# Performance work log

Hardware: AMD Instinct MI355X
Metric: run time of the kernel (lower is better)

## Reference

```python
import jax, jax.numpy as jnp
import numpy as np

NEG_INF_DIAG = 1000000.0

def setup_inputs() -> dict:
    key = jax.random.key(0)
    k1, k2, k3 = jax.random.split(key, 3)
    B, N, S, D = 64, 32, 256, 128
    return {
        "query_embeddings": jax.random.normal(k1, (B, N, D), dtype=jnp.float32),
        "doc_embeddings": jax.random.normal(k2, (B, S, D), dtype=jnp.float32),
        "neg_doc_embeddings": jax.random.normal(k3, (B, S, D), dtype=jnp.float32),
    }

def _maxsim(q, d):
    # q: (b, n, dim), d: (b, s, dim) -> (b,) sum over n of max over s of q.d
    return jnp.einsum('bnd,bsd->bns', q, d).max(axis=2).sum(axis=1)

def reference(query_embeddings, doc_embeddings, neg_doc_embeddings):
    pos_scores = _maxsim(query_embeddings, doc_embeddings)
    neg_scores = _maxsim(query_embeddings, neg_doc_embeddings)
    loss = jax.nn.softplus(neg_scores - pos_scores).mean()

    # in-batch term: scores[b, c] = MaxSim(query b, doc c)
    scores = jnp.einsum('bnd,csd->bcns', query_embeddings, doc_embeddings).max(axis=3).sum(axis=2)  # (B, B)
    pos = jnp.diagonal(scores)
    B = scores.shape[0]
    neg = (scores - jnp.eye(B, dtype=scores.dtype) * NEG_INF_DIAG).max(axis=1)
    loss = loss + jax.nn.softplus(neg - pos).mean()
    return loss / 2
```

## Files before the change

### kernel.cpp

```cpp
#include <hip/hip_runtime.h>
#include <hip/hip_bf16.h>

#define B_SZ 64
#define N_Q 32

typedef __attribute__((ext_vector_type(8))) short bf16x8;
typedef __attribute__((ext_vector_type(4))) float f32x4;

static __device__ __forceinline__ unsigned short f2bf(float f) {
    __hip_bfloat16 h = __float2bfloat16(f);
    return *reinterpret_cast<unsigned short*>(&h);
}

static __device__ __forceinline__ bf16x8 cvt_frag(const float* __restrict__ src) {
    float4 a = reinterpret_cast<const float4*>(src)[0];
    float4 b = reinterpret_cast<const float4*>(src)[1];
    union { bf16x8 v; unsigned short u[8]; } t;
    t.u[0] = f2bf(a.x); t.u[1] = f2bf(a.y); t.u[2] = f2bf(a.z); t.u[3] = f2bf(a.w);
    t.u[4] = f2bf(b.x); t.u[5] = f2bf(b.y); t.u[6] = f2bf(b.z); t.u[7] = f2bf(b.w);
    return t.v;
}

#define MFMA(A, Bv, C) __builtin_amdgcn_mfma_f32_16x16x32_bf16(A, Bv, C, 0, 0, 0)

__global__ __launch_bounds__(256) void cvt_permute(const float* __restrict__ q,
                                                   const float* __restrict__ dd,
                                                   const float* __restrict__ nd,
                                                   unsigned short* __restrict__ DP,
                                                   unsigned short* __restrict__ QP) {
    const int blk = blockIdx.x, tid = threadIdx.x;
    if (blk < 2048) {
        const int o = blk * 256 + tid;
        const int doc = o >> 12;
        const int u = o & 4095;
        const int ln = u & 63, nt = (u >> 6) & 3, kk = (u >> 8) & 3, ch = u >> 10;
        const int s  = ch * 64 + nt * 16 + (ln & 15);
        const int k0 = kk * 32 + (ln >> 4) * 8;
        const float* src = ((doc < 64) ? (dd + (size_t)doc * 32768)
                                       : (nd + (size_t)(doc - 64) * 32768)) + s * 128 + k0;
        reinterpret_cast<bf16x8*>(DP)[o] = cvt_frag(src);
    } else {
        const int g = (blk - 2048) * 256 + tid;
        const int b = g >> 9, u = g & 511;
        const int ln = u & 63, mt = (u >> 6) & 1, kk = u >> 7;
        const int n  = mt * 16 + (ln & 15);
        const int k0 = kk * 32 + (ln >> 4) * 8;
        reinterpret_cast<bf16x8*>(QP)[g] = cvt_frag(q + (size_t)b * 4096 + n * 128 + k0);
    }
}

__global__ __launch_bounds__(256, 2) void maxsim_kernel(const unsigned short* __restrict__ QP,
                                                        const unsigned short* __restrict__ DP,
                                                        float* __restrict__ scores) {
    const int wg  = blockIdx.x;
    const int tid = threadIdx.x;
    const int wave = tid >> 6, lane = tid & 63;
    const int l15 = lane & 15;

    __shared__ bf16x8 docB[4096];
    __shared__ float wredN[4][4][8];

    const bf16x8* DP8 = reinterpret_cast<const bf16x8*>(DP);
    const bf16x8* QP8 = reinterpret_cast<const bf16x8*>(QP);

    int c, b;
    bool isNeg;
    if (wg < 1024) { c = wg >> 4; b = (wg & 15) * 4 + wave; isNeg = false; }
    else           { b = wg - 1024; c = b; isNeg = true; }
    const int dcc = isNeg ? (64 + b) : c;

    bf16x8 Af[4][2];
    const bf16x8* qsrc = QP8 + (size_t)b * 512 + lane;
    #pragma unroll
    for (int kk = 0; kk < 4; ++kk) {
        Af[kk][0] = qsrc[kk * 128];
        Af[kk][1] = qsrc[kk * 128 + 64];
    }

    const bf16x8* dsrc = DP8 + (size_t)dcc * 4096 + wave * 1024 + lane;
    #pragma unroll
    for (int f = 0; f < 16; ++f)
        docB[wave * 1024 + f * 64 + lane] = dsrc[f * 64];
    __syncthreads();

    float rmax[2][4];
    #pragma unroll
    for (int mt = 0; mt < 2; ++mt)
        #pragma unroll
        for (int r = 0; r < 4; ++r) rmax[mt][r] = -3.0e38f;

    const int nch = isNeg ? 1 : 4;
    for (int i = 0; i < nch; ++i) {
        const int ch = isNeg ? wave : ((wave + i) & 3);
        f32x4 acc[2][4] = {};
        #pragma unroll
        for (int kk = 0; kk < 4; ++kk) {
            #pragma unroll
            for (int nt = 0; nt < 4; ++nt) {
                bf16x8 Bv = docB[ch * 1024 + kk * 256 + nt * 64 + lane];
                acc[0][nt] = MFMA(Af[kk][0], Bv, acc[0][nt]);
                acc[1][nt] = MFMA(Af[kk][1], Bv, acc[1][nt]);
            }
        }
        #pragma unroll
        for (int mt = 0; mt < 2; ++mt)
            #pragma unroll
            for (int r = 0; r < 4; ++r)
                rmax[mt][r] = fmaxf(rmax[mt][r],
                    fmaxf(fmaxf(acc[mt][0][r], acc[mt][1][r]),
                          fmaxf(acc[mt][2][r], acc[mt][3][r])));
    }

    float part = 0.0f;
    #pragma unroll
    for (int mt = 0; mt < 2; ++mt)
        #pragma unroll
        for (int r = 0; r < 4; ++r) {
            float m = rmax[mt][r];
            m = fmaxf(m, __shfl_xor(m, 1, 64));
            m = fmaxf(m, __shfl_xor(m, 2, 64));
            m = fmaxf(m, __shfl_xor(m, 4, 64));
            m = fmaxf(m, __shfl_xor(m, 8, 64));
            if (isNeg) {
                if (l15 == 0) wredN[wave][lane >> 4][mt * 4 + r] = m;
            } else {
                part += m;
            }
        }
    if (!isNeg) {
        part += __shfl_xor(part, 16, 64);
        part += __shfl_xor(part, 32, 64);
        if (lane == 0) scores[(size_t)b * 65 + c] = part;
    } else {
        __syncthreads();
        if (tid < 32) {
            const int l4v = tid >> 3, slot = tid & 7;
            float m = fmaxf(fmaxf(wredN[0][l4v][slot], wredN[1][l4v][slot]),
                            fmaxf(wredN[2][l4v][slot], wredN[3][l4v][slot]));
            m += __shfl_xor(m, 1, 64);
            m += __shfl_xor(m, 2, 64);
            m += __shfl_xor(m, 4, 64);
            m += __shfl_xor(m, 8, 64);
            m += __shfl_xor(m, 16, 64);
            if (tid == 0) scores[(size_t)b * 65 + 64] = m;
        }
    }
}

static __device__ __forceinline__ float softplusf(float x) {
    return fmaxf(x, 0.0f) + log1pf(expf(-fabsf(x)));
}

__global__ __launch_bounds__(64) void loss_kernel(const float* __restrict__ scores,
                                                  float* __restrict__ out) {
    const int b = threadIdx.x;
    const float* row = scores + b * 65;
    const float pos  = row[b];
    const float negq = row[64];
    float nib = -1e30f;
    #pragma unroll
    for (int c = 0; c < B_SZ; ++c) {
        float v = row[c] - ((c == b) ? 1000000.0f : 0.0f);
        nib = fmaxf(nib, v);
    }
    float t = softplusf(negq - pos) + softplusf(nib - pos);
    t += __shfl_xor(t, 1, 64);
    t += __shfl_xor(t, 2, 64);
    t += __shfl_xor(t, 4, 64);
    t += __shfl_xor(t, 8, 64);
    t += __shfl_xor(t, 16, 64);
    t += __shfl_xor(t, 32, 64);
    if (b == 0) out[0] = t * (0.5f / 64.0f);
}

extern "C" void kernel_launch(void* const* d_in, const int* in_sizes, int n_in,
                              void* d_out, int out_size, void* d_ws, size_t ws_size,
                              hipStream_t stream) {
    const float* q  = (const float*)d_in[0];
    const float* dd = (const float*)d_in[1];
    const float* nd = (const float*)d_in[2];
    float* out = (float*)d_out;

    unsigned short* DP = (unsigned short*)d_ws;
    unsigned short* QP = DP + (size_t)128 * 32768;
    float* scores = (float*)(QP + (size_t)64 * 4096);

    cvt_permute<<<2176, 256, 0, stream>>>(q, dd, nd, DP, QP);

    maxsim_kernel<<<1024 + B_SZ, 256, 0, stream>>>(QP, DP, scores);

    loss_kernel<<<1, 64, 0, stream>>>(scores, out);
}
```

Before: 88.18 us.

## Fuse fp32-to-bf16 conversion into maxsim kernel with two queries per wave

Drops the separate cvt_permute pass. The maxsim kernel now reads fp32 queries and documents directly, converts them to bf16 in registers and writes documents into a swizzled LDS layout. Each wave handles two queries, so the grid halves and every LDS doc fragment feeds twice as many MFMAs. The negative-doc blocks now run all four chunks redundantly per wave and keep only one result. Risks are uncoalesced strided fp32 loads, redundant conversion of the same document across 8 blocks, and higher register pressure.

```diff
diff --git a/kernel.cpp b/kernel.cpp
--- a/kernel.cpp
+++ b/kernel.cpp
@@ -2,7 +2,6 @@
 #include <hip/hip_bf16.h>
 
 #define B_SZ 64
-#define N_Q 32
 
 typedef __attribute__((ext_vector_type(8))) short bf16x8;
 typedef __attribute__((ext_vector_type(4))) float f32x4;
@@ -23,127 +22,105 @@
 
 #define MFMA(A, Bv, C) __builtin_amdgcn_mfma_f32_16x16x32_bf16(A, Bv, C, 0, 0, 0)
 
-__global__ __launch_bounds__(256) void cvt_permute(const float* __restrict__ q,
-                                                   const float* __restrict__ dd,
-                                                   const float* __restrict__ nd,
-                                                   unsigned short* __restrict__ DP,
-                                                   unsigned short* __restrict__ QP) {
-    const int blk = blockIdx.x, tid = threadIdx.x;
-    if (blk < 2048) {
-        const int o = blk * 256 + tid;
-        const int doc = o >> 12;
-        const int u = o & 4095;
-        const int ln = u & 63, nt = (u >> 6) & 3, kk = (u >> 8) & 3, ch = u >> 10;
-        const int s  = ch * 64 + nt * 16 + (ln & 15);
-        const int k0 = kk * 32 + (ln >> 4) * 8;
-        const float* src = ((doc < 64) ? (dd + (size_t)doc * 32768)
-                                       : (nd + (size_t)(doc - 64) * 32768)) + s * 128 + k0;
-        reinterpret_cast<bf16x8*>(DP)[o] = cvt_frag(src);
-    } else {
-        const int g = (blk - 2048) * 256 + tid;
-        const int b = g >> 9, u = g & 511;
-        const int ln = u & 63, mt = (u >> 6) & 1, kk = u >> 7;
-        const int n  = mt * 16 + (ln & 15);
-        const int k0 = kk * 32 + (ln >> 4) * 8;
-        reinterpret_cast<bf16x8*>(QP)[g] = cvt_frag(q + (size_t)b * 4096 + n * 128 + k0);
-    }
-}
-
-__global__ __launch_bounds__(256, 2) void maxsim_kernel(const unsigned short* __restrict__ QP,
-                                                        const unsigned short* __restrict__ DP,
+__global__ __launch_bounds__(256, 2) void maxsim_kernel(const float* __restrict__ q,
+                                                        const float* __restrict__ dd,
+                                                        const float* __restrict__ nd,
                                                         float* __restrict__ scores) {
-    const int wg  = blockIdx.x;
-    const int tid = threadIdx.x;
+    const int idx = blockIdx.x, tid = threadIdx.x;
     const int wave = tid >> 6, lane = tid & 63;
-    const int l15 = lane & 15;
+    const int l15 = lane & 15, l4 = lane >> 4;
 
     __shared__ bf16x8 docB[4096];
-    __shared__ float wredN[4][4][8];
 
-    const bf16x8* DP8 = reinterpret_cast<const bf16x8*>(DP);
-    const bf16x8* QP8 = reinterpret_cast<const bf16x8*>(QP);
-
-    int c, b;
-    bool isNeg;
-    if (wg < 1024) { c = wg >> 4; b = (wg & 15) * 4 + wave; isNeg = false; }
-    else           { b = wg - 1024; c = b; isNeg = true; }
-    const int dcc = isNeg ? (64 + b) : c;
-
-    bf16x8 Af[4][2];
-    const bf16x8* qsrc = QP8 + (size_t)b * 512 + lane;
-    #pragma unroll
-    for (int kk = 0; kk < 4; ++kk) {
-        Af[kk][0] = qsrc[kk * 128];
-        Af[kk][1] = qsrc[kk * 128 + 64];
+    int b0, b1, ccol;
+    const float* docf;
+    if (idx < 512) {
+        const int c = idx >> 3, g = idx & 7;
+        b0 = g * 8 + wave * 2; b1 = b0 + 1; ccol = c;
+        docf = dd + (size_t)c * 32768;
+    } else {
+        b0 = b1 = idx - 512; ccol = B_SZ;
+        docf = nd + (size_t)b0 * 32768;
     }
 
-    const bf16x8* dsrc = DP8 + (size_t)dcc * 4096 + wave * 1024 + lane;
+    bf16x8 Af[2][4][2];
     #pragma unroll
-    for (int f = 0; f < 16; ++f)
-        docB[wave * 1024 + f * 64 + lane] = dsrc[f * 64];
+    for (int kk = 0; kk < 4; ++kk)
+        #pragma unroll
+        for (int mt = 0; mt < 2; ++mt) {
+            const int off = (mt * 16 + l15) * 128 + kk * 32 + l4 * 8;
+            Af[0][kk][mt] = cvt_frag(q + (size_t)b0 * 4096 + off);
+            Af[1][kk][mt] = cvt_frag(q + (size_t)b1 * 4096 + off);
+        }
+
+    {
+        const float* dsrc = docf + wave * 8192;
+        #pragma unroll
+        for (int f = 0; f < 16; ++f) {
+            const int s_local = f * 4 + l4;
+            const int kc = l15;
+            bf16x8 v = cvt_frag(dsrc + s_local * 128 + kc * 8);
+            const int logical = wave * 1024 + (kc >> 2) * 256 + (s_local >> 4) * 64
+                                + (kc & 3) * 16 + (s_local & 15);
+            docB[logical ^ ((kc >> 2) << 1)] = v;
+        }
+    }
     __syncthreads();
 
-    float rmax[2][4];
+    float rmax[2][2][4];
     #pragma unroll
-    for (int mt = 0; mt < 2; ++mt)
+    for (int qi = 0; qi < 2; ++qi)
         #pragma unroll
-        for (int r = 0; r < 4; ++r) rmax[mt][r] = -3.0e38f;
+        for (int mt = 0; mt < 2; ++mt)
+            #pragma unroll
+            for (int r = 0; r < 4; ++r) rmax[qi][mt][r] = -3.0e38f;
 
-    const int nch = isNeg ? 1 : 4;
-    for (int i = 0; i < nch; ++i) {
-        const int ch = isNeg ? wave : ((wave + i) & 3);
-        f32x4 acc[2][4] = {};
+    #pragma unroll
+    for (int i = 0; i < 4; ++i) {
+        const int ch = (wave + i) & 3;
+        f32x4 acc[2][2][4] = {};
         #pragma unroll
         for (int kk = 0; kk < 4; ++kk) {
+            const int rbase = ch * 1024 + kk * 256 + (lane ^ (kk << 1));
             #pragma unroll
             for (int nt = 0; nt < 4; ++nt) {
-                bf16x8 Bv = docB[ch * 1024 + kk * 256 + nt * 64 + lane];
-                acc[0][nt] = MFMA(Af[kk][0], Bv, acc[0][nt]);
-                acc[1][nt] = MFMA(Af[kk][1], Bv, acc[1][nt]);
+                bf16x8 Bv = docB[rbase + nt * 64];
+                acc[0][0][nt] = MFMA(Af[0][kk][0], Bv, acc[0][0][nt]);
+                acc[0][1][nt] = MFMA(Af[0][kk][1], Bv, acc[0][1][nt]);
+                acc[1][0][nt] = MFMA(Af[1][kk][0], Bv, acc[1][0][nt]);
+                acc[1][1][nt] = MFMA(Af[1][kk][1], Bv, acc[1][1][nt]);
             }
         }
         #pragma unroll
+        for (int qi = 0; qi < 2; ++qi)
+            #pragma unroll
+            for (int mt = 0; mt < 2; ++mt)
+                #pragma unroll
+                for (int r = 0; r < 4; ++r)
+                    rmax[qi][mt][r] = fmaxf(rmax[qi][mt][r],
+                        fmaxf(fmaxf(acc[qi][mt][0][r], acc[qi][mt][1][r]),
+                              fmaxf(acc[qi][mt][2][r], acc[qi][mt][3][r])));
+    }
+
+    #pragma unroll
+    for (int qi = 0; qi < 2; ++qi) {
+        float part = 0.0f;
+        #pragma unroll
         for (int mt = 0; mt < 2; ++mt)
             #pragma unroll
-            for (int r = 0; r < 4; ++r)
-                rmax[mt][r] = fmaxf(rmax[mt][r],
-                    fmaxf(fmaxf(acc[mt][0][r], acc[mt][1][r]),
-                          fmaxf(acc[mt][2][r], acc[mt][3][r])));
-    }
-
-    float part = 0.0f;
-    #pragma unroll
-    for (int mt = 0; mt < 2; ++mt)
-        #pragma unroll
-        for (int r = 0; r < 4; ++r) {
-            float m = rmax[mt][r];
-            m = fmaxf(m, __shfl_xor(m, 1, 64));
-            m = fmaxf(m, __shfl_xor(m, 2, 64));
-            m = fmaxf(m, __shfl_xor(m, 4, 64));
-            m = fmaxf(m, __shfl_xor(m, 8, 64));
-            if (isNeg) {
-                if (l15 == 0) wredN[wave][lane >> 4][mt * 4 + r] = m;
-            } else {
+            for (int r = 0; r < 4; ++r) {
+                float m = rmax[qi][mt][r];
+                m = fmaxf(m, __shfl_xor(m, 1, 64));
+                m = fmaxf(m, __shfl_xor(m, 2, 64));
+                m = fmaxf(m, __shfl_xor(m, 4, 64));
+                m = fmaxf(m, __shfl_xor(m, 8, 64));
                 part += m;
             }
-        }
-    if (!isNeg) {
         part += __shfl_xor(part, 16, 64);
         part += __shfl_xor(part, 32, 64);
-        if (lane == 0) scores[(size_t)b * 65 + c] = part;
-    } else {
-        __syncthreads();
-        if (tid < 32) {
-            const int l4v = tid >> 3, slot = tid & 7;
-            float m = fmaxf(fmaxf(wredN[0][l4v][slot], wredN[1][l4v][slot]),
-                            fmaxf(wredN[2][l4v][slot], wredN[3][l4v][slot]));
-            m += __shfl_xor(m, 1, 64);
-            m += __shfl_xor(m, 2, 64);
-            m += __shfl_xor(m, 4, 64);
-            m += __shfl_xor(m, 8, 64);
-            m += __shfl_xor(m, 16, 64);
-            if (tid == 0) scores[(size_t)b * 65 + 64] = m;
-        }
+        const int b = qi ? b1 : b0;
+        if (lane == 0 && (idx < 512 ? true : (wave == 0 && qi == 0)))
+            scores[(size_t)b * 65 + ccol] = part;
     }
 }
 
@@ -181,13 +158,9 @@
     const float* nd = (const float*)d_in[2];
     float* out = (float*)d_out;
 
-    unsigned short* DP = (unsigned short*)d_ws;
-    unsigned short* QP = DP + (size_t)128 * 32768;
-    float* scores = (float*)(QP + (size_t)64 * 4096);
+    float* scores = (float*)d_ws;
 
-    cvt_permute<<<2176, 256, 0, stream>>>(q, dd, nd, DP, QP);
-
-    maxsim_kernel<<<1024 + B_SZ, 256, 0, stream>>>(QP, DP, scores);
+    maxsim_kernel<<<512 + B_SZ, 256, 0, stream>>>(q, dd, nd, scores);
 
     loss_kernel<<<1, 64, 0, stream>>>(scores, out);
 }
```

After: 109.1 us. 1.24x slower.
